# Optimization experiments

Measured on AMD Instinct MI355X. Metric: run time of the kernel, lower is better.

The kernel has to match this reference:

```python
import jax, jax.numpy as jnp
import numpy as np

NUM_CLASSES = 21
TOP_K = 200
CONF_THRESH = 0.01
NMS_THRESH = 0.045
VAR0, VAR1 = 0.1, 0.2  # SSD decode variances
B, N = 128, 8732  # batch, num anchors (SSD300)


def setup_inputs() -> dict:
    key = jax.random.key(0)
    k1, k2, k3 = jax.random.split(key, 3)
    loc = jax.random.normal(k1, (B, N, 4), jnp.float32)
    conf = jax.random.normal(k2, (B, N, NUM_CLASSES), jnp.float32)
    # anchors in center-size form (cx, cy, w, h), values in (0,1)
    anchors = jax.random.uniform(k3, (N, 4), jnp.float32)
    return {"loc": loc, "conf": conf, "anchors": anchors}


def decode(loc, anchors):
    # loc [N,4], anchors [N,4] (cx,cy,w,h) -> corner boxes [N,4]
    cxcy = anchors[:, :2] + loc[:, :2] * VAR0 * anchors[:, 2:]
    wh = anchors[:, 2:] * jnp.exp(loc[:, 2:] * VAR1)
    return jnp.concatenate([cxcy - 0.5 * wh, cxcy + 0.5 * wh], axis=-1)


def pairwise_iou(boxes):
    # boxes [K,4] -> IoU [K,K]
    lt = jnp.maximum(boxes[:, None, :2], boxes[None, :, :2])
    rb = jnp.minimum(boxes[:, None, 2:], boxes[None, :, 2:])
    wh = jnp.clip(rb - lt, 0.0)
    inter = wh[..., 0] * wh[..., 1]
    area = (boxes[:, 2] - boxes[:, 0]) * (boxes[:, 3] - boxes[:, 1])
    return inter / (area[:, None] + area[None, :] - inter + 1e-12)


def nms_one_class(scores, boxes):
    # scores [N], boxes [N,4] -> packed [TOP_K, 5] (score, x1,y1,x2,y2)
    masked = jnp.where(scores > CONF_THRESH, scores, 0.0)
    top_s, idx = jax.lax.top_k(masked, TOP_K)
    top_b = boxes[idx]                      # [K,4]
    iou = pairwise_iou(top_b)               # [K,K]
    ar = jnp.arange(TOP_K)
    def body(i, keep):
        sup = keep[i] & (iou[i] > NMS_THRESH) & (ar > i)
        return keep & ~sup
    keep = jax.lax.fori_loop(0, TOP_K, body, top_s > CONF_THRESH)
    # pack kept detections to the front (stable sort preserves score order)
    order = jnp.argsort(jnp.logical_not(keep))
    ent = jnp.concatenate([top_s[:, None], top_b], axis=-1)[order]
    return jnp.where(keep[order][:, None], ent, 0.0)


def reference(loc, conf, anchors):
    probs = jax.nn.softmax(conf, axis=-1)   # [B,N,C]
    def per_image(loc_i, probs_i):
        boxes = decode(loc_i, anchors)      # [N,4]
        return jax.vmap(lambda s: nms_one_class(s, boxes))(probs_i.T)  # [C,K,5]
    out = jax.vmap(per_image)(loc, probs)   # [B,C,K,5]
    return out.at[:, 0].set(0.0)            # class 0 = background, left zero
```

## Files before the change

kernel.cpp:

```cpp
#include <hip/hip_runtime.h>
#include <math.h>

#pragma clang fp contract(off)

#define NB 128
#define NA 8732
#define NAP 8736
#define NC 21
#define TOPK 200
#define BCAP 512
#define CONF_T 0.01
#define NMS_T 0.045
#define NV (NAP / 8)
#define HSIZE 904
#define CHN 226
#define CHPAD 232
#define CH2N 29
#define KSAMP 30

__device__ __forceinline__ double exact_score_cf(const float* __restrict__ conf,
                                                 int b, int i, int c) {
  const float* row = conf + ((size_t)b * NA + i) * NC;
  float r[NC];
#pragma unroll
  for (int k = 0; k < NC; ++k) r[k] = row[k];
  float mx = r[0];
#pragma unroll
  for (int k = 1; k < NC; ++k) mx = fmaxf(mx, r[k]);
  double d = 0.0;
#pragma unroll
  for (int k = 0; k < NC; ++k) d += exp((double)r[k] - (double)mx);
  double s = exp((double)r[c] - (double)mx) / d;
  return (s > CONF_T) ? s : 0.0;
}

__device__ __forceinline__ double exact_score_aux(const float* __restrict__ conf,
                                                  const float* __restrict__ mxa,
                                                  const double* __restrict__ da,
                                                  int b, int i, int c) {
  size_t r = (size_t)b * NA + i;
  double v = (double)conf[r * NC + c];
  double m = (double)mxa[r];
  double s = exp(v - m) / da[r];
  return (s > CONF_T) ? s : 0.0;
}

__device__ __forceinline__ double exact_score(const float* __restrict__ conf,
                                              const float* __restrict__ mxa,
                                              const double* __restrict__ da,
                                              int use_aux, int b, int i, int c) {
  if (use_aux) return exact_score_aux(conf, mxa, da, b, i, c);
  return exact_score_cf(conf, b, i, c);
}

__device__ __forceinline__ void decode64(const float* __restrict__ loc,
                                         const float* __restrict__ anchors,
                                         int b, int ai, double* o) {
  const float* lp = loc + ((size_t)b * NA + ai) * 4;
  const float* ap = anchors + (size_t)ai * 4;
  double l0 = (double)lp[0], l1 = (double)lp[1];
  double l2 = (double)lp[2], l3 = (double)lp[3];
  double a0 = (double)ap[0], a1 = (double)ap[1];
  double a2 = (double)ap[2], a3 = (double)ap[3];
  double cx = a0 + (l0 * 0.1) * a2;
  double cy = a1 + (l1 * 0.1) * a3;
  double w = a2 * exp(l2 * 0.2);
  double h = a3 * exp(l3 * 0.2);
  o[0] = cx - 0.5 * w; o[1] = cy - 0.5 * h;
  o[2] = cx + 0.5 * w; o[3] = cy + 0.5 * h;
}

__device__ __forceinline__ bool entBefore(double sa, int ia, double sb, int ib) {
  return (sa > sb) || (sa == sb && ia < ib);
}

__device__ __forceinline__ unsigned wave_suffix_sum(unsigned v, int lane) {
#pragma unroll
  for (int off = 1; off < 64; off <<= 1) {
    unsigned o = (unsigned)__shfl_down((int)v, off);
    v += (lane + off < 64) ? o : 0u;
  }
  return v;
}

__global__ __launch_bounds__(256) void k_prep(const float* __restrict__ conf,
                                              unsigned short* __restrict__ scores,
                                              float* __restrict__ mxout,
                                              double* __restrict__ dout,
                                              int do_aux) {
  __shared__ float rows[256 * NC];
  int base = blockIdx.x * 256;
  const float4* src = (const float4*)(conf + (size_t)base * NC);
  float4* dst = (float4*)rows;
  for (int t = threadIdx.x; t < (256 * NC) / 4; t += 256) dst[t] = src[t];
  __syncthreads();
  int g = base + threadIdx.x;
  const float* row = rows + threadIdx.x * NC;
  float v[NC];
#pragma unroll
  for (int k = 0; k < NC; ++k) v[k] = row[k];
  float mx = v[0];
#pragma unroll
  for (int k = 1; k < NC; ++k) mx = fmaxf(mx, v[k]);
  float e[NC], s = 0.0f;
#pragma unroll
  for (int k = 0; k < NC; ++k) {
    e[k] = expf(v[k] - mx);
    s += e[k];
  }
  float inv = 1.0f / s;
  int b = g / NA, i = g - b * NA;
#pragma unroll
  for (int cc = 1; cc < NC; ++cc) {
    float sc = e[cc] * inv;
    scores[(size_t)(b * (NC - 1) + (cc - 1)) * NAP + i] =
        (sc > 0.0099f) ? (unsigned short)(__float_as_uint(sc) >> 16)
                       : (unsigned short)0;
  }
  if (do_aux) {
    double d = 0.0;
#pragma unroll
    for (int k = 0; k < NC; ++k) d += exp((double)v[k] - (double)mx);
    mxout[g] = mx;
    dout[g] = d;
  }
}

__global__ __launch_bounds__(256) void k_pad(unsigned short* __restrict__ scores) {
  int r = blockIdx.x * 256 + threadIdx.x;
  if (r < NB * (NC - 1)) {
    unsigned short* p = scores + (size_t)r * NAP + NA;
    p[0] = 0; p[1] = 0; p[2] = 0; p[3] = 0;
  }
}

__global__ __launch_bounds__(256, 8) void k_fast(const float* __restrict__ loc,
                                                 const float* __restrict__ conf,
                                                 const float* __restrict__ anchors,
                                                 const unsigned short* __restrict__ scores,
                                                 const float* __restrict__ mxa,
                                                 const double* __restrict__ da,
                                                 float* __restrict__ out,
                                                 int use_aux) {
  int id = blockIdx.x;
  int xcd = id & 7, slot0 = id >> 3;
  int c = slot0 % NC;
  int b = (slot0 / NC) * 8 + xcd;
  int tid = threadIdx.x;
  float* outbase = out + ((size_t)(b * NC + c)) * TOPK * 5;

  if (c == 0) {
    for (int k = tid; k < TOPK * 5; k += 256) outbase[k] = 0.0f;
    return;
  }

  __shared__ unsigned hist[HSIZE];
  __shared__ unsigned chunk[CHPAD];
  __shared__ unsigned chunk2[32];
  union U2 {
    struct { double bnds[BCAP]; int bndi[BCAP]; } bb;
    double dbox[TOPK][4];
  };
  __shared__ U2 u2;
  union U3 {
    unsigned suf[HSIZE];
    struct { float4 fbox[TOPK]; float farea[TOPK]; } fb;
  };
  __shared__ U3 u3;
  __shared__ double ssel[256];
  __shared__ int isel[256];
  __shared__ unsigned keepw[7];
  __shared__ int ctl_cnt, ctl_m, ctl_n1, ctl_kneed, ctl_lo, ctl_hi, ctl_k;
  __shared__ int ctl_fix, ctl_redo;
  __shared__ unsigned ctl_pref, ctl_L;

  const unsigned short* srow =
      scores + (size_t)(b * (NC - 1) + (c - 1)) * NAP;
  const uint4* sv = (const uint4*)srow;

  for (int t = tid; t < TOPK; t += 256) isel[t] = 0;
  if (tid < 32) chunk2[tid] = 0u;
  if (tid == 0) { ctl_cnt = 0; ctl_m = 0; ctl_fix = 0; }
  __syncthreads();
  {
    unsigned k16 = srow[tid * 34];
    if (k16) {
      int x = (int)k16 - 0x3BFF;
      if (x < 1) x = 1;
      if (x > HSIZE - 1) x = HSIZE - 1;
      atomicAdd(&chunk2[x >> 5], 1u);
    }
  }
  __syncthreads();
  if (tid < 64) {
    unsigned h = (tid < CH2N) ? chunk2[tid] : 0u;
    unsigned s = wave_suffix_sum(h, tid);
    unsigned long long bal = __ballot((int)(tid < CH2N && s >= (unsigned)KSAMP));
    if (tid == 0) {
      int w = bal ? (63 - (int)__clzll(bal)) : -1;
      ctl_L = (w >= 1) ? (unsigned)(0x3BFF + (w << 5)) : 0u;
    }
  }
  __syncthreads();

  unsigned L16x = ctl_L ? ctl_L : 1u;
  int lo, hi, n1, kneed;
  for (;;) {
    for (int t = tid; t < HSIZE; t += 256) hist[t] = 0u;
    if (tid == 0) ctl_redo = 0;
    __syncthreads();
    for (int q = tid; q < NV; q += 256) {
      uint4 v = sv[q];
      unsigned ks[8] = {v.x & 0xFFFFu, v.x >> 16, v.y & 0xFFFFu, v.y >> 16,
                        v.z & 0xFFFFu, v.z >> 16, v.w & 0xFFFFu, v.w >> 16};
#pragma unroll
      for (int t = 0; t < 8; ++t) {
        if (ks[t] >= L16x) {
          int x = (int)ks[t] - 0x3BFF;
          if (x < 1) x = 1;
          if (x > HSIZE - 1) x = HSIZE - 1;
          atomicAdd(&hist[x], 1u);
        }
      }
    }
    __syncthreads();
    if (tid < CHN) {
      unsigned csum = 0;
#pragma unroll
      for (int j = 0; j < 4; ++j) csum += hist[tid * 4 + j];
      chunk[tid] = csum;
    } else if (tid < CHPAD) {
      chunk[tid] = 0u;
    }
    __syncthreads();
    if (tid < 64) {
      int lane = tid;
      unsigned h2 = 0;
      if (lane < CH2N) {
        int cb = lane * 8;
#pragma unroll
        for (int j = 0; j < 8; ++j) h2 += chunk[cb + j];
      }
      unsigned s2 = wave_suffix_sum(h2, lane);
      unsigned long long bal = __ballot((int)(lane < CH2N && s2 >= (unsigned)TOPK));
      int t2 = bal ? (63 - (int)__clzll(bal)) : -1;
      if (t2 < 0 && L16x > 1u) {
        if (lane == 0) ctl_redo = 1;
      } else {
        if (t2 < 0) {
          if (lane == 0) {
            ctl_lo = 1; ctl_hi = 0; ctl_n1 = (int)s2; ctl_kneed = TOPK - (int)s2;
          }
        } else {
          unsigned cumS = (unsigned)__shfl((int)(s2 - h2), t2);
          unsigned hc = (lane < 8) ? chunk[t2 * 8 + lane] : 0u;
          unsigned sc = wave_suffix_sum(hc, lane);
          unsigned long long balc =
              __ballot((int)(lane < 8 && cumS + sc >= (unsigned)TOPK));
          int jc = 63 - (int)__clzll(balc);
          int tc = t2 * 8 + jc;
          unsigned cumC = cumS + (unsigned)__shfl((int)(sc - hc), jc);
          unsigned hb = (lane < 4) ? hist[tc * 4 + lane] : 0u;
          unsigned sb = wave_suffix_sum(hb, lane);
          unsigned long long balb =
              __ballot((int)(lane < 4 && cumC + sb >= (unsigned)TOPK));
          int jb = 63 - (int)__clzll(balb);
          int D = tc * 4 + jb;
          unsigned cum = cumC + (unsigned)__shfl((int)(sb - hb), jb);
          int hi_ = (D + 1 < HSIZE) ? D + 1 : D;
          int lo_ = (D - 1 >= 1) ? D - 1 : D;
          unsigned hup = (hi_ > D) ? hist[hi_] : 0u;
          if (lane == 0) {
            ctl_lo = lo_; ctl_hi = hi_;
            ctl_n1 = (int)(cum - hup);
            ctl_kneed = TOPK - ctl_n1;
          }
        }
        if (lane < 32) chunk2[lane] = s2 - h2;
      }
    }
    __syncthreads();
    if (!ctl_redo) break;
    L16x = 1u;
  }
  lo = ctl_lo; hi = ctl_hi; n1 = ctl_n1; kneed = ctl_kneed;

  if (tid < CHN) {
    unsigned s = chunk2[tid >> 3];
    int ge = ((tid >> 3) + 1) << 3;
    for (int u = tid + 1; u < ge; ++u) s += chunk[u];
    int b0 = tid * 4;
    unsigned h3 = hist[b0 + 3], h2 = hist[b0 + 2], h1 = hist[b0 + 1];
    u3.suf[b0 + 3] = s;
    u3.suf[b0 + 2] = s + h3;
    u3.suf[b0 + 1] = s + h3 + h2;
    u3.suf[b0 + 0] = s + h3 + h2 + h1;
  }
  __syncthreads();

  {
    unsigned tC16 = (unsigned)(0x3C00 + hi);
    unsigned tB16 = (unsigned)(0x3BFF + lo);
    for (int q = tid; q < NV; q += 256) {
      uint4 v = sv[q];
      unsigned ks[8] = {v.x & 0xFFFFu, v.x >> 16, v.y & 0xFFFFu, v.y >> 16,
                        v.z & 0xFFFFu, v.z >> 16, v.w & 0xFFFFu, v.w >> 16};
#pragma unroll
      for (int t = 0; t < 8; ++t) {
        unsigned key = ks[t];
        if (key >= tC16) {
          int x = (int)key - 0x3BFF;
          if (x > HSIZE - 1) x = HSIZE - 1;
          int slot = (int)u3.suf[x] + (int)atomicSub(&hist[x], 1u) - 1;
          if (slot < TOPK) isel[slot] = (x << 16) | (q * 8 + t);
        } else if (key >= tB16) {
          int p = atomicAdd(&ctl_m, 1);
          if (p < BCAP) u2.bb.bndi[p] = q * 8 + t;
        }
      }
    }
  }
  __syncthreads();
  int m = (hi > 0) ? ctl_m : 0;

  if (hi > 0 && m > BCAP) {
    if (tid == 0) { ctl_k = TOPK; ctl_pref = 0u; }
    __syncthreads();
    for (int shift = 8; shift >= 0; shift -= 8) {
      hist[tid] = 0u;
      __syncthreads();
      unsigned pref = ctl_pref;
      for (int q = tid; q < NV; q += 256) {
        uint4 v = sv[q];
        unsigned ks[8] = {v.x & 0xFFFFu, v.x >> 16, v.y & 0xFFFFu, v.y >> 16,
                          v.z & 0xFFFFu, v.z >> 16, v.w & 0xFFFFu, v.w >> 16};
#pragma unroll
        for (int t = 0; t < 8; ++t) {
          unsigned key = ks[t];
          if (key == 0u) continue;
          bool match = (shift == 8) || ((key >> 8) == (pref >> 8));
          if (match) atomicAdd(&hist[(key >> shift) & 255u], 1u);
        }
      }
      __syncthreads();
      if (tid == 0) {
        int k = ctl_k;
        unsigned cum = 0;
        int d = 255;
        for (; d > 0; --d) {
          unsigned h = hist[d];
          if (cum + h >= (unsigned)k) break;
          cum += h;
        }
        ctl_k = k - (int)cum;
        ctl_pref = pref | ((unsigned)d << shift);
      }
      __syncthreads();
    }
    unsigned Tf = ctl_pref;
    kneed = ctl_k;
    n1 = TOPK - kneed;
    if (tid == 0) { ctl_cnt = 0; ctl_m = 0; }
    __syncthreads();
    for (int q = tid; q < NV; q += 256) {
      uint4 v = sv[q];
      unsigned ks[8] = {v.x & 0xFFFFu, v.x >> 16, v.y & 0xFFFFu, v.y >> 16,
                        v.z & 0xFFFFu, v.z >> 16, v.w & 0xFFFFu, v.w >> 16};
#pragma unroll
      for (int t = 0; t < 8; ++t) {
        unsigned key = ks[t];
        if (key > Tf) {
          int p = atomicAdd(&ctl_cnt, 1);
          if (p < 256) isel[p] = q * 8 + t;
        } else if (key == Tf) {
          int p = atomicAdd(&ctl_m, 1);
          if (p < BCAP) u2.bb.bndi[p] = q * 8 + t;
        }
      }
    }
    __syncthreads();
    m = ctl_m;
    if (m > BCAP) m = BCAP;
    for (int q = tid; q < m; q += 256)
      u2.bb.bnds[q] = exact_score(conf, mxa, da, use_aux, b, u2.bb.bndi[q], c);
    __syncthreads();
    for (int q = tid; q < m; q += 256) {
      double sq = u2.bb.bnds[q];
      int iq = u2.bb.bndi[q];
      int rank = 0;
      for (int r = 0; r < m; ++r)
        if (entBefore(u2.bb.bnds[r], u2.bb.bndi[r], sq, iq)) ++rank;
      if (rank < kneed) { isel[n1 + rank] = iq; ssel[n1 + rank] = sq; }
    }
    __syncthreads();
    if (tid < TOPK) {
      if (tid < n1) ssel[tid] = exact_score(conf, mxa, da, use_aux, b, isel[tid], c);
    } else {
      ssel[tid] = -1.0;
      isel[tid] = 0x7fffffff;
    }
    for (int kk = 2; kk <= 256; kk <<= 1) {
      for (int j = kk >> 1; j > 0; j >>= 1) {
        __syncthreads();
        int ixj = tid ^ j;
        if (ixj > tid) {
          double s1 = ssel[tid], s2 = ssel[ixj];
          int i1 = isel[tid], i2 = isel[ixj];
          bool up = ((tid & kk) == 0);
          bool sw = up ? entBefore(s2, i2, s1, i1) : entBefore(s1, i1, s2, i2);
          if (sw) {
            ssel[tid] = s2; ssel[ixj] = s1;
            isel[tid] = i2; isel[ixj] = i1;
          }
        }
      }
    }
    __syncthreads();
  } else {
    if (tid < n1)
      ssel[tid] = exact_score(conf, mxa, da, use_aux, b, isel[tid] & 0xFFFF, c);
    if (hi > 0) {
      for (int q = tid; q < m; q += 256)
        u2.bb.bnds[q] = exact_score(conf, mxa, da, use_aux, b, u2.bb.bndi[q], c);
    }
    __syncthreads();
    double myS = 0.0;
    int myI = 0, myPos = -1;
    if (tid < n1) {
      int packed = isel[tid];
      int bk = packed >> 16;
      myI = packed & 0xFFFF;
      myS = ssel[tid];
      int base = (int)u3.suf[bk];
      int len = (int)u3.suf[bk - 1] - base;
      int r = 0;
      for (int u = base; u < base + len; ++u) {
        if (u == tid) continue;
        double ps = ssel[u];
        int pI = isel[u] & 0xFFFF;
        if (entBefore(ps, pI, myS, myI)) ++r;
      }
      myPos = base + r;
    }
    if (hi > 0) {
      for (int q = tid; q < m; q += 256) {
        double sq = u2.bb.bnds[q];
        int iq = u2.bb.bndi[q];
        int rank = 0;
        for (int r = 0; r < m; ++r)
          if (entBefore(u2.bb.bnds[r], u2.bb.bndi[r], sq, iq)) ++rank;
        if (rank < kneed) { isel[n1 + rank] = iq; ssel[n1 + rank] = sq; }
      }
    } else {
      for (int j = n1 + tid; j < TOPK; j += 256) {
        isel[j] = j - n1;
        ssel[j] = 0.0;
      }
    }
    __syncthreads();
    if (myPos >= 0 && myPos < TOPK) { ssel[myPos] = myS; isel[myPos] = myI; }
    __syncthreads();
    if (tid < 64) {
      bool inv = false;
      for (int j = tid + 1; j < TOPK; j += 64)
        if (entBefore(ssel[j], isel[j], ssel[j - 1], isel[j - 1])) inv = true;
      unsigned long long bal = __ballot((int)inv);
      if (tid == 0 && bal != 0ull) ctl_fix = 1;
    }
    __syncthreads();
    if (ctl_fix) {
      if (tid == 0) {
        for (int a = 1; a < TOPK; ++a) {
          double s = ssel[a];
          int ii = isel[a];
          int p = a - 1;
          while (p >= 0 && entBefore(s, ii, ssel[p], isel[p])) {
            ssel[p + 1] = ssel[p]; isel[p + 1] = isel[p]; --p;
          }
          ssel[p + 1] = s; isel[p + 1] = ii;
        }
      }
      __syncthreads();
    }
  }

  double dx1 = 0, dy1 = 0, dx2 = 0, dy2 = 0;
  if (tid < TOPK) {
    double bx[4];
    decode64(loc, anchors, b, isel[tid], bx);
    dx1 = bx[0]; dy1 = bx[1]; dx2 = bx[2]; dy2 = bx[3];
    u3.fb.fbox[tid] = make_float4((float)dx1, (float)dy1, (float)dx2, (float)dy2);
    u3.fb.farea[tid] = (float)((dx2 - dx1) * (dy2 - dy1));
    u2.dbox[tid][0] = dx1; u2.dbox[tid][1] = dy1;
    u2.dbox[tid][2] = dx2; u2.dbox[tid][3] = dy2;
  }
  __syncthreads();

  if (tid < 64) {
    int l = tid;
    unsigned kr = 0u;
    float4 ob[4]; float oa[4];
#pragma unroll
    for (int q = 0; q < 4; ++q) {
      int j = l + 64 * q;
      if (j < TOPK) {
        if (ssel[j] > CONF_T) kr |= 1u << q;
        ob[q] = u3.fb.fbox[j];
        oa[q] = u3.fb.farea[j];
      } else {
        ob[q] = make_float4(0.0f, 0.0f, 0.0f, 0.0f);
        oa[q] = 0.0f;
      }
    }
    int cur = 0;
    while (cur < TOPK) {
      unsigned long long ms0 = __ballot((int)(kr & 1u));
      unsigned long long ms1 = __ballot((int)(kr & 2u));
      unsigned long long ms2 = __ballot((int)(kr & 4u));
      unsigned long long ms3 = __ballot((int)(kr & 8u));
      int q0 = cur >> 6;
      int sh = cur & 63;
      unsigned long long below = sh ? ((1ull << sh) - 1ull) : 0ull;
      unsigned long long t0 = (q0 == 0) ? (ms0 & ~below) : 0ull;
      unsigned long long t1 = (q0 < 1) ? ms1 : ((q0 == 1) ? (ms1 & ~below) : 0ull);
      unsigned long long t2 = (q0 < 2) ? ms2 : ((q0 == 2) ? (ms2 & ~below) : 0ull);
      unsigned long long t3 = (q0 < 3) ? ms3 : (ms3 & ~below);
      int i = TOPK;
      if (t0) i = __ffsll(t0) - 1;
      else if (t1) i = 64 + __ffsll(t1) - 1;
      else if (t2) i = 128 + __ffsll(t2) - 1;
      else if (t3) i = 192 + __ffsll(t3) - 1;
      if (i >= TOPK) break;
      float4 fbi = u3.fb.fbox[i];
      float fai = u3.fb.farea[i];
#pragma unroll
      for (int q = 0; q < 4; ++q) {
        int r = l + 64 * q;
        if (r > i && r < TOPK && ((kr >> q) & 1u)) {
          float lx = fmaxf(fbi.x, ob[q].x), ly = fmaxf(fbi.y, ob[q].y);
          float rx = fminf(fbi.z, ob[q].z), ry = fminf(fbi.w, ob[q].w);
          float iw = fmaxf(rx - lx, 0.0f), ih = fmaxf(ry - ly, 0.0f);
          float inter = iw * ih;
          float uni = fai + oa[q] - inter + 1e-12f;
          float diff = inter - 0.045f * uni;
          bool sup;
          if (fabsf(diff) < 3e-4f * uni) {
            double ix1 = u2.dbox[i][0], iy1 = u2.dbox[i][1];
            double ix2 = u2.dbox[i][2], iy2 = u2.dbox[i][3];
            double jx1 = u2.dbox[r][0], jy1 = u2.dbox[r][1];
            double jx2 = u2.dbox[r][2], jy2 = u2.dbox[r][3];
            double dlx = fmax(ix1, jx1), dly = fmax(iy1, jy1);
            double drx = fmin(ix2, jx2), dry = fmin(iy2, jy2);
            double diw = drx - dlx; if (diw < 0.0) diw = 0.0;
            double dih = dry - dly; if (dih < 0.0) dih = 0.0;
            double dint = diw * dih;
            double dai = (ix2 - ix1) * (iy2 - iy1);
            double daj = (jx2 - jx1) * (jy2 - jy1);
            sup = dint > NMS_T * (dai + daj - dint + 1e-12);
          } else {
            sup = diff > 0.0f;
          }
          if (sup) kr &= ~(1u << q);
        }
      }
      cur = i + 1;
    }
#pragma unroll
    for (int q = 0; q < 4; ++q) {
      unsigned long long bal = __ballot((int)((kr >> q) & 1u));
      if (l == 0) {
        keepw[2 * q] = (unsigned)bal;
        if (2 * q + 1 < 7) keepw[2 * q + 1] = (unsigned)(bal >> 32);
      }
    }
  }
  __syncthreads();

  int nk = 0;
#pragma unroll
  for (int w = 0; w < 7; ++w) nk += __popc(keepw[w]);
  if (tid < TOPK) {
    int j = tid;
    bool kept = (keepw[j >> 5] >> (j & 31)) & 1u;
    if (kept) {
      int pos = 0;
      for (int w = 0; w < (j >> 5); ++w) pos += __popc(keepw[w]);
      pos += __popc(keepw[j >> 5] & ((1u << (j & 31)) - 1u));
      float* o = outbase + (size_t)pos * 5;
      o[0] = (float)ssel[j];
      o[1] = (float)dx1;
      o[2] = (float)dy1;
      o[3] = (float)dx2;
      o[4] = (float)dy2;
    }
    if (j >= nk) {
      float* o = outbase + (size_t)j * 5;
      o[0] = 0.0f; o[1] = 0.0f; o[2] = 0.0f; o[3] = 0.0f; o[4] = 0.0f;
    }
  }
}

__global__ __launch_bounds__(256) void k_main_nf(const float* __restrict__ loc,
                                                 const float* __restrict__ conf,
                                                 const float* __restrict__ anchors,
                                                 float* __restrict__ out) {
  int bc = blockIdx.x;
  int b = bc / NC;
  int c = bc % NC;
  int tid = threadIdx.x;
  float* outbase = out + (size_t)bc * TOPK * 5;
  if (c == 0) {
    for (int k = tid; k < TOPK * 5; k += 256) outbase[k] = 0.0f;
    return;
  }
  union U {
    float sf[NA];
    struct { double box[TOPK][4]; double area[TOPK]; } p2;
  };
  __shared__ U u;
  __shared__ double ssel[256];
  __shared__ int isel[256];
  __shared__ unsigned hist[256];
  __shared__ double bnds[256];
  __shared__ int bndi[256];
  __shared__ int keepL[256];
  __shared__ unsigned long long wmask[4];
  __shared__ int ctl_k, ctl_cnt, ctl_m;
  __shared__ unsigned ctl_pref;

  for (int i = tid; i < NA; i += 256)
    u.sf[i] = (float)exact_score_cf(conf, b, i, c);
  if (tid == 0) { ctl_k = TOPK; ctl_pref = 0u; }
  __syncthreads();
  for (int shift = 24; shift >= 0; shift -= 8) {
    hist[tid] = 0u;
    __syncthreads();
    unsigned pref = ctl_pref;
    for (int i = tid; i < NA; i += 256) {
      unsigned key = __float_as_uint(u.sf[i]);
      bool match = (shift == 24) || ((key >> (shift + 8)) == (pref >> (shift + 8)));
      if (match) atomicAdd(&hist[(key >> shift) & 255u], 1u);
    }
    __syncthreads();
    if (tid == 0) {
      int k = ctl_k;
      unsigned cum = 0;
      int d = 255;
      for (; d > 0; --d) {
        unsigned h = hist[d];
        if (cum + h >= (unsigned)k) break;
        cum += h;
      }
      ctl_k = k - (int)cum;
      ctl_pref = pref | ((unsigned)d << shift);
    }
    __syncthreads();
  }
  unsigned Tf = ctl_pref;
  int kneed = ctl_k;
  int n1 = TOPK - kneed;
  if (tid == 0) { ctl_cnt = 0; ctl_m = 0; }
  __syncthreads();
  for (int i = tid; i < NA; i += 256) {
    unsigned key = __float_as_uint(u.sf[i]);
    if (key > Tf) {
      int p = atomicAdd(&ctl_cnt, 1);
      if (p < 256) isel[p] = i;
    } else if (key == Tf && Tf != 0u) {
      int q = atomicAdd(&ctl_m, 1);
      if (q < 256) bndi[q] = i;
    }
  }
  __syncthreads();
  int zf;
  if (Tf == 0u) {
    zf = n1;
    for (int j = n1 + tid; j < TOPK; j += 256) isel[j] = j - n1;
  } else {
    zf = TOPK;
    int m = ctl_m;
    if (m > 256) m = 256;
    if (tid < m) bnds[tid] = exact_score_cf(conf, b, bndi[tid], c);
    __syncthreads();
    if (tid < m) {
      double sq = bnds[tid];
      int iq = bndi[tid];
      int rank = 0;
      for (int r = 0; r < m; ++r)
        if (entBefore(bnds[r], bndi[r], sq, iq)) ++rank;
      if (rank < kneed) isel[n1 + rank] = iq;
    }
  }
  __syncthreads();
  if (tid < TOPK) {
    ssel[tid] = (tid < zf) ? exact_score_cf(conf, b, isel[tid], c) : 0.0;
  } else {
    ssel[tid] = -1.0;
    isel[tid] = 0x7fffffff;
  }
  for (int kk = 2; kk <= 256; kk <<= 1) {
    for (int j = kk >> 1; j > 0; j >>= 1) {
      __syncthreads();
      int ixj = tid ^ j;
      if (ixj > tid) {
        double s1 = ssel[tid], s2 = ssel[ixj];
        int i1 = isel[tid], i2 = isel[ixj];
        bool up = ((tid & kk) == 0);
        bool sw = up ? entBefore(s2, i2, s1, i1) : entBefore(s1, i1, s2, i2);
        if (sw) {
          ssel[tid] = s2; ssel[ixj] = s1;
          isel[tid] = i2; isel[ixj] = i1;
        }
      }
    }
  }
  __syncthreads();
  if (tid < TOPK) {
    double bx[4];
    decode64(loc, anchors, b, isel[tid], bx);
    u.p2.box[tid][0] = bx[0]; u.p2.box[tid][1] = bx[1];
    u.p2.box[tid][2] = bx[2]; u.p2.box[tid][3] = bx[3];
    u.p2.area[tid] = (bx[2] - bx[0]) * (bx[3] - bx[1]);
  }
  __syncthreads();
  double mx1 = 0, my1 = 0, mx2 = 0, my2 = 0, mar = 0;
  if (tid < TOPK) {
    mx1 = u.p2.box[tid][0]; my1 = u.p2.box[tid][1];
    mx2 = u.p2.box[tid][2]; my2 = u.p2.box[tid][3];
    mar = u.p2.area[tid];
  }
  keepL[tid] = (tid < TOPK) && (ssel[tid] > CONF_T);
  __syncthreads();
  for (int i = 0; i < TOPK; ++i) {
    int ki = keepL[i];
    if (ki && tid > i && tid < TOPK && keepL[tid]) {
      double lx = fmax(u.p2.box[i][0], mx1);
      double ly = fmax(u.p2.box[i][1], my1);
      double rx = fmin(u.p2.box[i][2], mx2);
      double ry = fmin(u.p2.box[i][3], my2);
      double iw = rx - lx; if (iw < 0.0) iw = 0.0;
      double ih = ry - ly; if (ih < 0.0) ih = 0.0;
      double inter = iw * ih;
      double iou = inter / (u.p2.area[i] + mar - inter + 1e-12);
      if (iou > NMS_T) keepL[tid] = 0;
    }
    __syncthreads();
  }
  bool kj = (tid < TOPK) && (keepL[tid] != 0);
  unsigned long long bal = __ballot((int)kj);
  int wave = tid >> 6, lane = tid & 63;
  if (lane == 0) wmask[wave] = bal;
  __syncthreads();
  int nk = 0;
#pragma unroll
  for (int w = 0; w < 4; ++w) nk += __popcll(wmask[w]);
  if (kj) {
    int pos = 0;
    for (int w = 0; w < wave; ++w) pos += __popcll(wmask[w]);
    pos += __popcll(bal & ((1ull << lane) - 1ull));
    float* o = outbase + (size_t)pos * 5;
    o[0] = (float)ssel[tid];
    o[1] = (float)u.p2.box[tid][0];
    o[2] = (float)u.p2.box[tid][1];
    o[3] = (float)u.p2.box[tid][2];
    o[4] = (float)u.p2.box[tid][3];
  }
  if (tid < TOPK && tid >= nk) {
    float* o = outbase + (size_t)tid * 5;
    o[0] = 0.0f; o[1] = 0.0f; o[2] = 0.0f; o[3] = 0.0f; o[4] = 0.0f;
  }
}

extern "C" void kernel_launch(void* const* d_in, const int* in_sizes, int n_in,
                              void* d_out, int out_size, void* d_ws, size_t ws_size,
                              hipStream_t stream) {
  const float* loc = (const float*)d_in[0];
  const float* conf = (const float*)d_in[1];
  const float* anchors = (const float*)d_in[2];
  float* out = (float*)d_out;

  const size_t SC_BYTES = (size_t)NB * (NC - 1) * NAP * sizeof(unsigned short);
  const size_t MX_BYTES = (size_t)NB * NA * sizeof(float);
  const size_t D_BYTES = (size_t)NB * NA * sizeof(double);

  if (ws_size >= SC_BYTES + MX_BYTES + D_BYTES) {
    unsigned short* scores = (unsigned short*)d_ws;
    float* mxa = (float*)((char*)d_ws + SC_BYTES);
    double* da = (double*)((char*)d_ws + SC_BYTES + MX_BYTES);
    k_pad<<<10, 256, 0, stream>>>(scores);
    k_prep<<<(NB * NA) / 256, 256, 0, stream>>>(conf, scores, mxa, da, 1);
    k_fast<<<NB * NC, 256, 0, stream>>>(loc, conf, anchors, scores, mxa, da, out, 1);
  } else if (ws_size >= SC_BYTES) {
    unsigned short* scores = (unsigned short*)d_ws;
    k_pad<<<10, 256, 0, stream>>>(scores);
    k_prep<<<(NB * NA) / 256, 256, 0, stream>>>(conf, scores, nullptr, nullptr, 0);
    k_fast<<<NB * NC, 256, 0, stream>>>(loc, conf, anchors, scores, nullptr, nullptr, out, 0);
  } else {
    k_main_nf<<<NB * NC, 256, 0, stream>>>(loc, conf, anchors, out);
  }
}
```

Baseline: 116.6 us.

## Cache threshold candidates in LDS to skip second score scan, slim aux and LDS

The first histogram pass now also records every key at or above a sampled floor into an LDS candidate list. When the list fits, the second selection pass walks that list instead of rescanning the whole score row from global memory. The softmax max and denominator are packed into one double2 per anchor, and the background-class zeroing moves into k_pad so k_fast launches only the 20 real classes. Box decode switches to float, and the double-precision boxes are recomputed from global memory only for borderline IoU cases, freeing LDS. The sample doubles to raise the floor's accuracy, and an extra redo path triggers when the floor lies above the chosen bin; the candidate atomics add contention to the first pass.

```diff
diff --git a/kernel.cpp b/kernel.cpp
--- a/kernel.cpp
+++ b/kernel.cpp
@@ -9,6 +9,7 @@
 #define NC 21
 #define TOPK 200
 #define BCAP 512
+#define CANDCAP 1024
 #define CONF_T 0.01
 #define NMS_T 0.045
 #define NV (NAP / 8)
@@ -16,7 +17,7 @@
 #define CHN 226
 #define CHPAD 232
 #define CH2N 29
-#define KSAMP 30
+#define KSAMP 40
 
 __device__ __forceinline__ double exact_score_cf(const float* __restrict__ conf,
                                                  int b, int i, int c) {
@@ -35,21 +36,19 @@
 }
 
 __device__ __forceinline__ double exact_score_aux(const float* __restrict__ conf,
-                                                  const float* __restrict__ mxa,
-                                                  const double* __restrict__ da,
+                                                  const double2* __restrict__ aux,
                                                   int b, int i, int c) {
   size_t r = (size_t)b * NA + i;
   double v = (double)conf[r * NC + c];
-  double m = (double)mxa[r];
-  double s = exp(v - m) / da[r];
+  double2 a = aux[r];
+  double s = exp(v - a.y) / a.x;
   return (s > CONF_T) ? s : 0.0;
 }
 
 __device__ __forceinline__ double exact_score(const float* __restrict__ conf,
-                                              const float* __restrict__ mxa,
-                                              const double* __restrict__ da,
+                                              const double2* __restrict__ aux,
                                               int use_aux, int b, int i, int c) {
-  if (use_aux) return exact_score_aux(conf, mxa, da, b, i, c);
+  if (use_aux) return exact_score_aux(conf, aux, b, i, c);
   return exact_score_cf(conf, b, i, c);
 }
 
@@ -85,8 +84,7 @@
 
 __global__ __launch_bounds__(256) void k_prep(const float* __restrict__ conf,
                                               unsigned short* __restrict__ scores,
-                                              float* __restrict__ mxout,
-                                              double* __restrict__ dout,
+                                              double2* __restrict__ aux,
                                               int do_aux) {
   __shared__ float rows[256 * NC];
   int base = blockIdx.x * 256;
@@ -121,15 +119,20 @@
     double d = 0.0;
 #pragma unroll
     for (int k = 0; k < NC; ++k) d += exp((double)v[k] - (double)mx);
-    mxout[g] = mx;
-    dout[g] = d;
-  }
-}
-
-__global__ __launch_bounds__(256) void k_pad(unsigned short* __restrict__ scores) {
-  int r = blockIdx.x * 256 + threadIdx.x;
-  if (r < NB * (NC - 1)) {
-    unsigned short* p = scores + (size_t)r * NAP + NA;
+    aux[g] = make_double2(d, (double)mx);
+  }
+}
+
+__global__ __launch_bounds__(256) void k_pad(unsigned short* __restrict__ scores,
+                                             float* __restrict__ out) {
+  int t = blockIdx.x * 256 + threadIdx.x;
+  if (t < NB * TOPK * 5) {
+    int bb = t / (TOPK * 5);
+    int r = t - bb * (TOPK * 5);
+    out[(size_t)bb * NC * TOPK * 5 + r] = 0.0f;
+  }
+  if (t < NB * (NC - 1)) {
+    unsigned short* p = scores + (size_t)t * NAP + NA;
     p[0] = 0; p[1] = 0; p[2] = 0; p[3] = 0;
   }
 }
@@ -138,28 +141,22 @@
                                                  const float* __restrict__ conf,
                                                  const float* __restrict__ anchors,
                                                  const unsigned short* __restrict__ scores,
-                                                 const float* __restrict__ mxa,
-                                                 const double* __restrict__ da,
+                                                 const double2* __restrict__ aux,
                                                  float* __restrict__ out,
                                                  int use_aux) {
   int id = blockIdx.x;
   int xcd = id & 7, slot0 = id >> 3;
-  int c = slot0 % NC;
-  int b = (slot0 / NC) * 8 + xcd;
+  int c = 1 + (slot0 % (NC - 1));
+  int b = (slot0 / (NC - 1)) * 8 + xcd;
   int tid = threadIdx.x;
   float* outbase = out + ((size_t)(b * NC + c)) * TOPK * 5;
-
-  if (c == 0) {
-    for (int k = tid; k < TOPK * 5; k += 256) outbase[k] = 0.0f;
-    return;
-  }
 
   __shared__ unsigned hist[HSIZE];
   __shared__ unsigned chunk[CHPAD];
   __shared__ unsigned chunk2[32];
   union U2 {
+    unsigned cand[CANDCAP];
     struct { double bnds[BCAP]; int bndi[BCAP]; } bb;
-    double dbox[TOPK][4];
   };
   __shared__ U2 u2;
   union U3 {
@@ -170,7 +167,7 @@
   __shared__ double ssel[256];
   __shared__ int isel[256];
   __shared__ unsigned keepw[7];
-  __shared__ int ctl_cnt, ctl_m, ctl_n1, ctl_kneed, ctl_lo, ctl_hi, ctl_k;
+  __shared__ int ctl_cnt, ctl_m, ctl_n1, ctl_kneed, ctl_lo, ctl_hi, ctl_k, ctl_c;
   __shared__ int ctl_fix, ctl_redo;
   __shared__ unsigned ctl_pref, ctl_L;
 
@@ -183,9 +180,16 @@
   if (tid == 0) { ctl_cnt = 0; ctl_m = 0; ctl_fix = 0; }
   __syncthreads();
   {
-    unsigned k16 = srow[tid * 34];
-    if (k16) {
-      int x = (int)k16 - 0x3BFF;
+    unsigned s0 = srow[tid * 34];
+    unsigned s1 = srow[tid * 34 + 17];
+    if (s0) {
+      int x = (int)s0 - 0x3BFF;
+      if (x < 1) x = 1;
+      if (x > HSIZE - 1) x = HSIZE - 1;
+      atomicAdd(&chunk2[x >> 5], 1u);
+    }
+    if (s1) {
+      int x = (int)s1 - 0x3BFF;
       if (x < 1) x = 1;
       if (x > HSIZE - 1) x = HSIZE - 1;
       atomicAdd(&chunk2[x >> 5], 1u);
@@ -203,11 +207,11 @@
   }
   __syncthreads();
 
-  unsigned L16x = ctl_L ? ctl_L : 1u;
+  unsigned F16 = ctl_L ? (ctl_L - 1u) : 1u;
   int lo, hi, n1, kneed;
   for (;;) {
     for (int t = tid; t < HSIZE; t += 256) hist[t] = 0u;
-    if (tid == 0) ctl_redo = 0;
+    if (tid == 0) { ctl_redo = 0; ctl_c = 0; }
     __syncthreads();
     for (int q = tid; q < NV; q += 256) {
       uint4 v = sv[q];
@@ -215,11 +219,13 @@
                         v.z & 0xFFFFu, v.z >> 16, v.w & 0xFFFFu, v.w >> 16};
 #pragma unroll
       for (int t = 0; t < 8; ++t) {
-        if (ks[t] >= L16x) {
+        if (ks[t] >= F16) {
           int x = (int)ks[t] - 0x3BFF;
           if (x < 1) x = 1;
           if (x > HSIZE - 1) x = HSIZE - 1;
           atomicAdd(&hist[x], 1u);
+          int p = atomicAdd(&ctl_c, 1);
+          if (p < CANDCAP) u2.cand[p] = (ks[t] << 16) | (unsigned)(q * 8 + t);
         }
       }
     }
@@ -244,7 +250,7 @@
       unsigned s2 = wave_suffix_sum(h2, lane);
       unsigned long long bal = __ballot((int)(lane < CH2N && s2 >= (unsigned)TOPK));
       int t2 = bal ? (63 - (int)__clzll(bal)) : -1;
-      if (t2 < 0 && L16x > 1u) {
+      if (t2 < 0 && F16 > 1u) {
         if (lane == 0) ctl_redo = 1;
       } else {
         if (t2 < 0) {
@@ -270,10 +276,15 @@
           int hi_ = (D + 1 < HSIZE) ? D + 1 : D;
           int lo_ = (D - 1 >= 1) ? D - 1 : D;
           unsigned hup = (hi_ > D) ? hist[hi_] : 0u;
+          int xF = (F16 > 1u) ? (int)(F16 - 0x3BFFu) : 1;
           if (lane == 0) {
-            ctl_lo = lo_; ctl_hi = hi_;
-            ctl_n1 = (int)(cum - hup);
-            ctl_kneed = TOPK - ctl_n1;
+            if (lo_ < xF && F16 > 1u) {
+              ctl_redo = 1;
+            } else {
+              ctl_lo = lo_; ctl_hi = hi_;
+              ctl_n1 = (int)(cum - hup);
+              ctl_kneed = TOPK - ctl_n1;
+            }
           }
         }
         if (lane < 32) chunk2[lane] = s2 - h2;
@@ -281,9 +292,12 @@
     }
     __syncthreads();
     if (!ctl_redo) break;
-    L16x = 1u;
+    F16 = 1u;
   }
   lo = ctl_lo; hi = ctl_hi; n1 = ctl_n1; kneed = ctl_kneed;
+  int ccnt = ctl_c;
+  bool cand_ok = (ccnt <= CANDCAP);
+  if (ccnt > CANDCAP) ccnt = CANDCAP;
 
   if (tid < CHN) {
     unsigned s = chunk2[tid >> 3];
@@ -301,21 +315,38 @@
   {
     unsigned tC16 = (unsigned)(0x3C00 + hi);
     unsigned tB16 = (unsigned)(0x3BFF + lo);
-    for (int q = tid; q < NV; q += 256) {
-      uint4 v = sv[q];
-      unsigned ks[8] = {v.x & 0xFFFFu, v.x >> 16, v.y & 0xFFFFu, v.y >> 16,
-                        v.z & 0xFFFFu, v.z >> 16, v.w & 0xFFFFu, v.w >> 16};
-#pragma unroll
-      for (int t = 0; t < 8; ++t) {
-        unsigned key = ks[t];
+    if (cand_ok) {
+      for (int p = tid; p < ccnt; p += 256) {
+        unsigned e = u2.cand[p];
+        unsigned key = e >> 16;
+        int idx = (int)(e & 0xFFFFu);
         if (key >= tC16) {
           int x = (int)key - 0x3BFF;
           if (x > HSIZE - 1) x = HSIZE - 1;
           int slot = (int)u3.suf[x] + (int)atomicSub(&hist[x], 1u) - 1;
-          if (slot < TOPK) isel[slot] = (x << 16) | (q * 8 + t);
+          if (slot < TOPK) isel[slot] = (x << 16) | idx;
         } else if (key >= tB16) {
-          int p = atomicAdd(&ctl_m, 1);
-          if (p < BCAP) u2.bb.bndi[p] = q * 8 + t;
+          int p2 = atomicAdd(&ctl_m, 1);
+          if (p2 < BCAP) u2.bb.bndi[p2] = idx;
+        }
+      }
+    } else {
+      for (int q = tid; q < NV; q += 256) {
+        uint4 v = sv[q];
+        unsigned ks[8] = {v.x & 0xFFFFu, v.x >> 16, v.y & 0xFFFFu, v.y >> 16,
+                          v.z & 0xFFFFu, v.z >> 16, v.w & 0xFFFFu, v.w >> 16};
+#pragma unroll
+        for (int t = 0; t < 8; ++t) {
+          unsigned key = ks[t];
+          if (key >= tC16) {
+            int x = (int)key - 0x3BFF;
+            if (x > HSIZE - 1) x = HSIZE - 1;
+            int slot = (int)u3.suf[x] + (int)atomicSub(&hist[x], 1u) - 1;
+            if (slot < TOPK) isel[slot] = (x << 16) | (q * 8 + t);
+          } else if (key >= tB16) {
+            int p2 = atomicAdd(&ctl_m, 1);
+            if (p2 < BCAP) u2.bb.bndi[p2] = q * 8 + t;
+          }
         }
       }
     }
@@ -382,7 +413,7 @@
     m = ctl_m;
     if (m > BCAP) m = BCAP;
     for (int q = tid; q < m; q += 256)
-      u2.bb.bnds[q] = exact_score(conf, mxa, da, use_aux, b, u2.bb.bndi[q], c);
+      u2.bb.bnds[q] = exact_score(conf, aux, use_aux, b, u2.bb.bndi[q], c);
     __syncthreads();
     for (int q = tid; q < m; q += 256) {
       double sq = u2.bb.bnds[q];
@@ -394,7 +425,7 @@
     }
     __syncthreads();
     if (tid < TOPK) {
-      if (tid < n1) ssel[tid] = exact_score(conf, mxa, da, use_aux, b, isel[tid], c);
+      if (tid < n1) ssel[tid] = exact_score(conf, aux, use_aux, b, isel[tid], c);
     } else {
       ssel[tid] = -1.0;
       isel[tid] = 0x7fffffff;
@@ -418,10 +449,10 @@
     __syncthreads();
   } else {
     if (tid < n1)
-      ssel[tid] = exact_score(conf, mxa, da, use_aux, b, isel[tid] & 0xFFFF, c);
+      ssel[tid] = exact_score(conf, aux, use_aux, b, isel[tid] & 0xFFFF, c);
     if (hi > 0) {
       for (int q = tid; q < m; q += 256)
-        u2.bb.bnds[q] = exact_score(conf, mxa, da, use_aux, b, u2.bb.bndi[q], c);
+        u2.bb.bnds[q] = exact_score(conf, aux, use_aux, b, u2.bb.bndi[q], c);
     }
     __syncthreads();
     double myS = 0.0;
@@ -484,15 +515,21 @@
     }
   }
 
-  double dx1 = 0, dy1 = 0, dx2 = 0, dy2 = 0;
+  float fx1 = 0, fy1 = 0, fx2 = 0, fy2 = 0;
   if (tid < TOPK) {
-    double bx[4];
-    decode64(loc, anchors, b, isel[tid], bx);
-    dx1 = bx[0]; dy1 = bx[1]; dx2 = bx[2]; dy2 = bx[3];
-    u3.fb.fbox[tid] = make_float4((float)dx1, (float)dy1, (float)dx2, (float)dy2);
-    u3.fb.farea[tid] = (float)((dx2 - dx1) * (dy2 - dy1));
-    u2.dbox[tid][0] = dx1; u2.dbox[tid][1] = dy1;
-    u2.dbox[tid][2] = dx2; u2.dbox[tid][3] = dy2;
+    int ai = isel[tid];
+    const float* lp = loc + ((size_t)b * NA + ai) * 4;
+    const float* ap = anchors + (size_t)ai * 4;
+    float l0 = lp[0], l1 = lp[1], l2 = lp[2], l3 = lp[3];
+    float a0 = ap[0], a1 = ap[1], a2 = ap[2], a3 = ap[3];
+    float cx = a0 + (l0 * 0.1f) * a2;
+    float cy = a1 + (l1 * 0.1f) * a3;
+    float w = a2 * expf(l2 * 0.2f);
+    float h = a3 * expf(l3 * 0.2f);
+    fx1 = cx - 0.5f * w; fy1 = cy - 0.5f * h;
+    fx2 = cx + 0.5f * w; fy2 = cy + 0.5f * h;
+    u3.fb.fbox[tid] = make_float4(fx1, fy1, fx2, fy2);
+    u3.fb.farea[tid] = (fx2 - fx1) * (fy2 - fy1);
   }
   __syncthreads();
 
@@ -545,17 +582,16 @@
           float diff = inter - 0.045f * uni;
           bool sup;
           if (fabsf(diff) < 3e-4f * uni) {
-            double ix1 = u2.dbox[i][0], iy1 = u2.dbox[i][1];
-            double ix2 = u2.dbox[i][2], iy2 = u2.dbox[i][3];
-            double jx1 = u2.dbox[r][0], jy1 = u2.dbox[r][1];
-            double jx2 = u2.dbox[r][2], jy2 = u2.dbox[r][3];
-            double dlx = fmax(ix1, jx1), dly = fmax(iy1, jy1);
-            double drx = fmin(ix2, jx2), dry = fmin(iy2, jy2);
+            double bi[4], bj[4];
+            decode64(loc, anchors, b, isel[i], bi);
+            decode64(loc, anchors, b, isel[r], bj);
+            double dlx = fmax(bi[0], bj[0]), dly = fmax(bi[1], bj[1]);
+            double drx = fmin(bi[2], bj[2]), dry = fmin(bi[3], bj[3]);
             double diw = drx - dlx; if (diw < 0.0) diw = 0.0;
             double dih = dry - dly; if (dih < 0.0) dih = 0.0;
             double dint = diw * dih;
-            double dai = (ix2 - ix1) * (iy2 - iy1);
-            double daj = (jx2 - jx1) * (jy2 - jy1);
+            double dai = (bi[2] - bi[0]) * (bi[3] - bi[1]);
+            double daj = (bj[2] - bj[0]) * (bj[3] - bj[1]);
             sup = dint > NMS_T * (dai + daj - dint + 1e-12);
           } else {
             sup = diff > 0.0f;
@@ -588,10 +624,10 @@
       pos += __popc(keepw[j >> 5] & ((1u << (j & 31)) - 1u));
       float* o = outbase + (size_t)pos * 5;
       o[0] = (float)ssel[j];
-      o[1] = (float)dx1;
-      o[2] = (float)dy1;
-      o[3] = (float)dx2;
-      o[4] = (float)dy2;
+      o[1] = fx1;
+      o[2] = fy1;
+      o[3] = fx2;
+      o[4] = fy2;
     }
     if (j >= nk) {
       float* o = outbase + (size_t)j * 5;
@@ -780,21 +816,19 @@
   float* out = (float*)d_out;
 
   const size_t SC_BYTES = (size_t)NB * (NC - 1) * NAP * sizeof(unsigned short);
-  const size_t MX_BYTES = (size_t)NB * NA * sizeof(float);
-  const size_t D_BYTES = (size_t)NB * NA * sizeof(double);
-
-  if (ws_size >= SC_BYTES + MX_BYTES + D_BYTES) {
+  const size_t AUX_BYTES = (size_t)NB * NA * sizeof(double2);
+
+  if (ws_size >= SC_BYTES + AUX_BYTES) {
     unsigned short* scores = (unsigned short*)d_ws;
-    float* mxa = (float*)((char*)d_ws + SC_BYTES);
-    double* da = (double*)((char*)d_ws + SC_BYTES + MX_BYTES);
-    k_pad<<<10, 256, 0, stream>>>(scores);
-    k_prep<<<(NB * NA) / 256, 256, 0, stream>>>(conf, scores, mxa, da, 1);
-    k_fast<<<NB * NC, 256, 0, stream>>>(loc, conf, anchors, scores, mxa, da, out, 1);
+    double2* aux = (double2*)((char*)d_ws + SC_BYTES);
+    k_pad<<<(NB * TOPK * 5 + 255) / 256, 256, 0, stream>>>(scores, out);
+    k_prep<<<(NB * NA) / 256, 256, 0, stream>>>(conf, scores, aux, 1);
+    k_fast<<<NB * (NC - 1), 256, 0, stream>>>(loc, conf, anchors, scores, aux, out, 1);
   } else if (ws_size >= SC_BYTES) {
     unsigned short* scores = (unsigned short*)d_ws;
-    k_pad<<<10, 256, 0, stream>>>(scores);
-    k_prep<<<(NB * NA) / 256, 256, 0, stream>>>(conf, scores, nullptr, nullptr, 0);
-    k_fast<<<NB * NC, 256, 0, stream>>>(loc, conf, anchors, scores, nullptr, nullptr, out, 0);
+    k_pad<<<(NB * TOPK * 5 + 255) / 256, 256, 0, stream>>>(scores, out);
+    k_prep<<<(NB * NA) / 256, 256, 0, stream>>>(conf, scores, nullptr, 0);
+    k_fast<<<NB * (NC - 1), 256, 0, stream>>>(loc, conf, anchors, scores, nullptr, out, 0);
   } else {
     k_main_nf<<<NB * NC, 256, 0, stream>>>(loc, conf, anchors, out);
   }
```

Result: slower. 131.0 us (+12.4%).
